# Optimization experiments

Measured on AMD Instinct MI355X. Metric: run time of the kernel, lower is better.

The kernel has to match this reference:

```python
import jax, jax.numpy as jnp
import numpy as np

SCALING = 2.0  # lora alpha / r

def setup_inputs() -> dict:
    key = jax.random.key(0)
    k1, k2, k3, k4, k5 = jax.random.split(key, 5)
    B, S, D_IN, D_OUT, R = 4, 2048, 4096, 4096, 16
    x = jax.random.normal(k1, (B, S, D_IN), dtype=jnp.float32)
    weight = jax.random.normal(k2, (D_OUT, D_IN), dtype=jnp.float32) * 0.02
    lora_A = jax.random.normal(k3, (R, D_IN), dtype=jnp.float32) * (1.0 / np.sqrt(D_IN))
    lora_B = jax.random.normal(k4, (D_OUT, R), dtype=jnp.float32) * 0.02
    bias = jax.random.normal(k5, (D_OUT,), dtype=jnp.float32) * 0.02
    return {"x": x, "weight": weight, "lora_A": lora_A, "lora_B": lora_B, "bias": bias}

def reference(x, weight, lora_A, lora_B, bias):
    # Faithful to the torch module: materialize W + scaling * (B @ A), then F.linear.
    # effective_weight: [d_out, d_in]
    effective_weight = weight + SCALING * (lora_B @ lora_A)
    # F.linear(x, W, b) = x @ W.T + b
    out = jnp.einsum('bsd,od->bso', x, effective_weight) + bias
    return out
```

## Files before the change

kernel.cpp:

```cpp
#include <hip/hip_runtime.h>
#include <hip/hip_bf16.h>
#include <stdint.h>

typedef unsigned short u16;
typedef u16 u16x4 __attribute__((ext_vector_type(4)));
typedef short bf16x8 __attribute__((ext_vector_type(8)));
typedef float f32x4 __attribute__((ext_vector_type(4)));

__device__ __forceinline__ u16 f2bf(float f) {
  union { float f; uint32_t u; } v; v.f = f;
  uint32_t u = v.u;
  return (u16)((u + 0x7fffu + ((u >> 16) & 1u)) >> 16);
}

__global__ __launch_bounds__(256) void cvt_x_kernel(const float4* __restrict__ in,
                                                    u16x4* __restrict__ out, int n4) {
  int i = blockIdx.x * 256 + threadIdx.x;
  const int stride = gridDim.x * 256;
  for (; i < n4; i += stride) {
    float4 v = in[i];
    u16x4 o;
    o.x = f2bf(v.x); o.y = f2bf(v.y); o.z = f2bf(v.z); o.w = f2bf(v.w);
    out[i] = o;
  }
}

__global__ __launch_bounds__(256) void weff_kernel(const float* __restrict__ W,
                                                   const float* __restrict__ A,
                                                   const float* __restrict__ Bl,
                                                   u16* __restrict__ Wout, int DIN) {
  const int n = blockIdx.x;
  float bv[16];
#pragma unroll
  for (int r = 0; r < 16; ++r) bv[r] = 2.0f * Bl[n * 16 + r];
  const int iters = DIN / (256 * 4);
  for (int c = 0; c < iters; ++c) {
    const int k = (c * 256 + (int)threadIdx.x) * 4;
    float4 wv = *(const float4*)&W[(size_t)n * DIN + k];
#pragma unroll
    for (int r = 0; r < 16; ++r) {
      const float4 av = *(const float4*)&A[(size_t)r * DIN + k];
      wv.x += bv[r] * av.x;
      wv.y += bv[r] * av.y;
      wv.z += bv[r] * av.z;
      wv.w += bv[r] * av.w;
    }
    u16x4 o;
    o.x = f2bf(wv.x); o.y = f2bf(wv.y); o.z = f2bf(wv.z); o.w = f2bf(wv.w);
    *(u16x4*)&Wout[(size_t)n * DIN + k] = o;
  }
}

#define BM 256
#define BN 256

__global__ __launch_bounds__(512, 2) void gemm256_kernel(
    const u16* __restrict__ A, const u16* __restrict__ B,
    const float* __restrict__ bias, float* __restrict__ C,
    int M, int N, int K) {
  extern __shared__ u16 lds[];

  const int tid  = threadIdx.x;
  const int lane = tid & 63;
  const int wid  = tid >> 6;

  const int nwg = gridDim.x;
  const int cpx = nwg >> 3;
  const int f   = ((int)blockIdx.x & 7) * cpx + ((int)blockIdx.x >> 3);
  const int nbx = N / BN;
  const int bx = f % nbx, by = f / nbx;
  const int bm = by * BM, bn = bx * BN;

  const int wmL = (wid >> 2) * 128;
  const int wnL = (wid & 3) * 64;
  const int lr  = lane & 15;
  const int lk  = lane >> 4;
  const int rslot = ((lk ^ ((lr >> 1) & 3)) << 3);

  const int srow  = tid >> 2;
  const int sslot = (((tid & 3) ^ ((tid >> 3) & 3)) << 3);
  const u16* gA = A + (size_t)(bm + srow) * K + sslot;
  const u16* gB = B + (size_t)(bn + srow) * K + sslot;

  auto stageA = [&](int par, int ks, int kt) {
    u16* d = &lds[(par * 2 + ks) * 8192 + wid * 512];
    const u16* s = gA + kt * 64 + ks * 32;
#pragma unroll
    for (int i = 0; i < 2; ++i)
      __builtin_amdgcn_global_load_lds(
          (__attribute__((address_space(1))) const void*)(s + (size_t)i * 128 * K),
          (__attribute__((address_space(3))) void*)(d + i * 4096), 16, 0, 0);
  };
  auto stageB = [&](int par, int ks, int kt) {
    u16* d = &lds[32768 + (par * 2 + ks) * 8192 + wid * 512];
    const u16* s = gB + kt * 64 + ks * 32;
#pragma unroll
    for (int i = 0; i < 2; ++i)
      __builtin_amdgcn_global_load_lds(
          (__attribute__((address_space(1))) const void*)(s + (size_t)i * 128 * K),
          (__attribute__((address_space(3))) void*)(d + i * 4096), 16, 0, 0);
  };

  f32x4 acc[8][4];
#pragma unroll
  for (int i = 0; i < 8; ++i)
#pragma unroll
    for (int n = 0; n < 4; ++n) acc[i][n] = f32x4{0.f, 0.f, 0.f, 0.f};

  const int NT = K >> 6;
  stageA(0, 0, 0); stageB(0, 0, 0); stageA(0, 1, 0); stageB(0, 1, 0);

#define GATE4() do { asm volatile("s_waitcnt vmcnt(4)" ::: "memory"); \
                     __builtin_amdgcn_s_barrier(); } while (0)

  for (int t = 0; t < NT; ++t) {
    const int par = t & 1, npar = par ^ 1;
    const int tn = (t + 1 < NT) ? t + 1 : 0;

    auto ldA = [&](int ks, int mf) -> bf16x8 {
      return *(const bf16x8*)&lds[(par * 2 + ks) * 8192 + (wmL + mf * 16 + lr) * 32 + rslot];
    };
    auto ldB = [&](int ks, int nf) -> bf16x8 {
      return *(const bf16x8*)&lds[32768 + (par * 2 + ks) * 8192 + (wnL + nf * 16 + lr) * 32 + rslot];
    };

    bf16x8 a[4], b0[4], b1[4];

    GATE4();
#pragma unroll
    for (int n = 0; n < 4; ++n) b0[n] = ldB(0, n);
#pragma unroll
    for (int i = 0; i < 4; ++i) a[i] = ldA(0, i);
    stageA(npar, 0, tn);
    __builtin_amdgcn_s_setprio(1);
#pragma unroll
    for (int i = 0; i < 4; ++i)
#pragma unroll
      for (int n = 0; n < 4; ++n)
        acc[i][n] = __builtin_amdgcn_mfma_f32_16x16x32_bf16(a[i], b0[n], acc[i][n], 0, 0, 0);
    __builtin_amdgcn_s_setprio(0);

#pragma unroll
    for (int i = 0; i < 4; ++i) a[i] = ldA(0, 4 + i);
    stageB(npar, 0, tn);
    __builtin_amdgcn_s_setprio(1);
#pragma unroll
    for (int i = 0; i < 4; ++i)
#pragma unroll
      for (int n = 0; n < 4; ++n)
        acc[4 + i][n] = __builtin_amdgcn_mfma_f32_16x16x32_bf16(a[i], b0[n], acc[4 + i][n], 0, 0, 0);
    __builtin_amdgcn_s_setprio(0);

    GATE4();
#pragma unroll
    for (int n = 0; n < 4; ++n) b1[n] = ldB(1, n);
#pragma unroll
    for (int i = 0; i < 4; ++i) a[i] = ldA(1, i);
    stageA(npar, 1, tn);
    __builtin_amdgcn_s_setprio(1);
#pragma unroll
    for (int i = 0; i < 4; ++i)
#pragma unroll
      for (int n = 0; n < 4; ++n)
        acc[i][n] = __builtin_amdgcn_mfma_f32_16x16x32_bf16(a[i], b1[n], acc[i][n], 0, 0, 0);
    __builtin_amdgcn_s_setprio(0);

#pragma unroll
    for (int i = 0; i < 4; ++i) a[i] = ldA(1, 4 + i);
    stageB(npar, 1, tn);
    __builtin_amdgcn_s_setprio(1);
#pragma unroll
    for (int i = 0; i < 4; ++i)
#pragma unroll
      for (int n = 0; n < 4; ++n)
        acc[4 + i][n] = __builtin_amdgcn_mfma_f32_16x16x32_bf16(a[i], b1[n], acc[4 + i][n], 0, 0, 0);
    __builtin_amdgcn_s_setprio(0);
  }

  asm volatile("s_waitcnt vmcnt(0)" ::: "memory");
  __builtin_amdgcn_s_barrier();

#pragma unroll
  for (int nf = 0; nf < 4; ++nf) {
    const int col = bn + wnL + nf * 16 + lr;
    const float bv = bias[col];
#pragma unroll
    for (int mf = 0; mf < 8; ++mf) {
      const int row = bm + wmL + mf * 16 + lk * 4;
#pragma unroll
      for (int j = 0; j < 4; ++j)
        C[(size_t)(row + j) * N + col] = acc[mf][nf][j] + bv;
    }
  }
}

extern "C" void kernel_launch(void* const* d_in, const int* in_sizes, int n_in,
                              void* d_out, int out_size, void* d_ws, size_t ws_size,
                              hipStream_t stream) {
  const float* x  = (const float*)d_in[0];
  const float* w  = (const float*)d_in[1];
  const float* lA = (const float*)d_in[2];
  const float* lB = (const float*)d_in[3];
  const float* bs = (const float*)d_in[4];
  float* out = (float*)d_out;

  const int DOUT = in_sizes[4];
  const int DIN  = in_sizes[1] / DOUT;
  const int M    = in_sizes[0] / DIN;

  u16* Xb = (u16*)d_ws;
  u16* Wb = Xb + (size_t)M * DIN;

  const int n4 = (M * DIN) / 4;
  cvt_x_kernel<<<2048, 256, 0, stream>>>((const float4*)x, (u16x4*)Xb, n4);
  weff_kernel<<<DOUT, 256, 0, stream>>>(w, lA, lB, Wb, DIN);

  static bool attr_set = false;
  (void)hipFuncSetAttribute((const void*)gemm256_kernel,
                            hipFuncAttributeMaxDynamicSharedMemorySize, 131072);

  const int nwg = (M / BM) * (DOUT / BN);
  gemm256_kernel<<<nwg, 512, 131072, stream>>>(Xb, Wb, bs, out, M, DOUT, DIN);
}
```

Baseline: 342.3 us.

## Merge prep kernels and restructure GEMM barrier schedule per sub-phase

Merges the x-to-bf16 conversion and effective-weight kernels into one launch, with blocks split by index, to remove a launch and let the two prep tasks run concurrently. In the GEMM main loop, it replaces the two vmcnt-gated barriers per k-tile with a barrier after every LDS-read/stage group and after every MFMA cluster, plus an lgkmcnt(0) wait before each MFMA block. The intent is to keep waves in lockstep so MFMA and memory phases interleave better across waves. The cost is many more barriers per iteration, which could add stalls.

```diff
diff --git a/kernel.cpp b/kernel.cpp
--- a/kernel.cpp
+++ b/kernel.cpp
@@ -13,41 +13,40 @@
   return (u16)((u + 0x7fffu + ((u >> 16) & 1u)) >> 16);
 }
 
-__global__ __launch_bounds__(256) void cvt_x_kernel(const float4* __restrict__ in,
-                                                    u16x4* __restrict__ out, int n4) {
-  int i = blockIdx.x * 256 + threadIdx.x;
-  const int stride = gridDim.x * 256;
-  for (; i < n4; i += stride) {
-    float4 v = in[i];
-    u16x4 o;
-    o.x = f2bf(v.x); o.y = f2bf(v.y); o.z = f2bf(v.z); o.w = f2bf(v.w);
-    out[i] = o;
-  }
-}
-
-__global__ __launch_bounds__(256) void weff_kernel(const float* __restrict__ W,
-                                                   const float* __restrict__ A,
-                                                   const float* __restrict__ Bl,
-                                                   u16* __restrict__ Wout, int DIN) {
-  const int n = blockIdx.x;
-  float bv[16];
-#pragma unroll
-  for (int r = 0; r < 16; ++r) bv[r] = 2.0f * Bl[n * 16 + r];
-  const int iters = DIN / (256 * 4);
-  for (int c = 0; c < iters; ++c) {
-    const int k = (c * 256 + (int)threadIdx.x) * 4;
-    float4 wv = *(const float4*)&W[(size_t)n * DIN + k];
-#pragma unroll
-    for (int r = 0; r < 16; ++r) {
-      const float4 av = *(const float4*)&A[(size_t)r * DIN + k];
-      wv.x += bv[r] * av.x;
-      wv.y += bv[r] * av.y;
-      wv.z += bv[r] * av.z;
-      wv.w += bv[r] * av.w;
+__global__ __launch_bounds__(256) void aux_kernel(
+    const float4* __restrict__ x, u16x4* __restrict__ xb, int n4, int nCvt,
+    const float* __restrict__ W, const float* __restrict__ A,
+    const float* __restrict__ Bl, u16* __restrict__ Wout, int DIN) {
+  if ((int)blockIdx.x < nCvt) {
+    int i = blockIdx.x * 256 + threadIdx.x;
+    const int stride = nCvt * 256;
+    for (; i < n4; i += stride) {
+      float4 v = x[i];
+      u16x4 o;
+      o.x = f2bf(v.x); o.y = f2bf(v.y); o.z = f2bf(v.z); o.w = f2bf(v.w);
+      xb[i] = o;
     }
-    u16x4 o;
-    o.x = f2bf(wv.x); o.y = f2bf(wv.y); o.z = f2bf(wv.z); o.w = f2bf(wv.w);
-    *(u16x4*)&Wout[(size_t)n * DIN + k] = o;
+  } else {
+    const int n = blockIdx.x - nCvt;
+    float bv[16];
+#pragma unroll
+    for (int r = 0; r < 16; ++r) bv[r] = 2.0f * Bl[n * 16 + r];
+    const int iters = DIN / (256 * 4);
+    for (int c = 0; c < iters; ++c) {
+      const int k = (c * 256 + (int)threadIdx.x) * 4;
+      float4 wv = *(const float4*)&W[(size_t)n * DIN + k];
+#pragma unroll
+      for (int r = 0; r < 16; ++r) {
+        const float4 av = *(const float4*)&A[(size_t)r * DIN + k];
+        wv.x += bv[r] * av.x;
+        wv.y += bv[r] * av.y;
+        wv.z += bv[r] * av.z;
+        wv.w += bv[r] * av.w;
+      }
+      u16x4 o;
+      o.x = f2bf(wv.x); o.y = f2bf(wv.y); o.z = f2bf(wv.z); o.w = f2bf(wv.w);
+      *(u16x4*)&Wout[(size_t)n * DIN + k] = o;
+    }
   }
 }
 
@@ -109,9 +108,13 @@
 
   const int NT = K >> 6;
   stageA(0, 0, 0); stageB(0, 0, 0); stageA(0, 1, 0); stageB(0, 1, 0);
-
-#define GATE4() do { asm volatile("s_waitcnt vmcnt(4)" ::: "memory"); \
-                     __builtin_amdgcn_s_barrier(); } while (0)
+  asm volatile("s_waitcnt vmcnt(4)" ::: "memory");
+  __builtin_amdgcn_s_barrier();
+
+#define PIN()   asm volatile("" ::: "memory")
+#define LGKM0() asm volatile("s_waitcnt lgkmcnt(0)" ::: "memory")
+#define VM4()   asm volatile("s_waitcnt vmcnt(4)" ::: "memory")
+#define BAR()   __builtin_amdgcn_s_barrier()
 
   for (int t = 0; t < NT; ++t) {
     const int par = t & 1, npar = par ^ 1;
@@ -126,12 +129,12 @@
 
     bf16x8 a[4], b0[4], b1[4];
 
-    GATE4();
 #pragma unroll
     for (int n = 0; n < 4; ++n) b0[n] = ldB(0, n);
 #pragma unroll
     for (int i = 0; i < 4; ++i) a[i] = ldA(0, i);
     stageA(npar, 0, tn);
+    PIN(); BAR(); LGKM0();
     __builtin_amdgcn_s_setprio(1);
 #pragma unroll
     for (int i = 0; i < 4; ++i)
@@ -139,10 +142,12 @@
       for (int n = 0; n < 4; ++n)
         acc[i][n] = __builtin_amdgcn_mfma_f32_16x16x32_bf16(a[i], b0[n], acc[i][n], 0, 0, 0);
     __builtin_amdgcn_s_setprio(0);
+    BAR();
 
 #pragma unroll
     for (int i = 0; i < 4; ++i) a[i] = ldA(0, 4 + i);
     stageB(npar, 0, tn);
+    PIN(); BAR(); LGKM0();
     __builtin_amdgcn_s_setprio(1);
 #pragma unroll
     for (int i = 0; i < 4; ++i)
@@ -150,13 +155,15 @@
       for (int n = 0; n < 4; ++n)
         acc[4 + i][n] = __builtin_amdgcn_mfma_f32_16x16x32_bf16(a[i], b0[n], acc[4 + i][n], 0, 0, 0);
     __builtin_amdgcn_s_setprio(0);
-
-    GATE4();
+    VM4();
+    BAR();
+
 #pragma unroll
     for (int n = 0; n < 4; ++n) b1[n] = ldB(1, n);
 #pragma unroll
     for (int i = 0; i < 4; ++i) a[i] = ldA(1, i);
     stageA(npar, 1, tn);
+    PIN(); BAR(); LGKM0();
     __builtin_amdgcn_s_setprio(1);
 #pragma unroll
     for (int i = 0; i < 4; ++i)
@@ -164,10 +171,12 @@
       for (int n = 0; n < 4; ++n)
         acc[i][n] = __builtin_amdgcn_mfma_f32_16x16x32_bf16(a[i], b1[n], acc[i][n], 0, 0, 0);
     __builtin_amdgcn_s_setprio(0);
+    BAR();
 
 #pragma unroll
     for (int i = 0; i < 4; ++i) a[i] = ldA(1, 4 + i);
     stageB(npar, 1, tn);
+    PIN(); BAR(); LGKM0();
     __builtin_amdgcn_s_setprio(1);
 #pragma unroll
     for (int i = 0; i < 4; ++i)
@@ -175,6 +184,8 @@
       for (int n = 0; n < 4; ++n)
         acc[4 + i][n] = __builtin_amdgcn_mfma_f32_16x16x32_bf16(a[i], b1[n], acc[4 + i][n], 0, 0, 0);
     __builtin_amdgcn_s_setprio(0);
+    VM4();
+    BAR();
   }
 
   asm volatile("s_waitcnt vmcnt(0)" ::: "memory");
@@ -192,6 +203,10 @@
         C[(size_t)(row + j) * N + col] = acc[mf][nf][j] + bv;
     }
   }
+#undef PIN
+#undef LGKM0
+#undef VM4
+#undef BAR
 }
 
 extern "C" void kernel_launch(void* const* d_in, const int* in_sizes, int n_in,
@@ -212,10 +227,10 @@
   u16* Wb = Xb + (size_t)M * DIN;
 
   const int n4 = (M * DIN) / 4;
-  cvt_x_kernel<<<2048, 256, 0, stream>>>((const float4*)x, (u16x4*)Xb, n4);
-  weff_kernel<<<DOUT, 256, 0, stream>>>(w, lA, lB, Wb, DIN);
-
-  static bool attr_set = false;
+  const int nCvt = 2048;
+  aux_kernel<<<nCvt + DOUT, 256, 0, stream>>>((const float4*)x, (u16x4*)Xb, n4, nCvt,
+                                              w, lA, lB, Wb, DIN);
+
   (void)hipFuncSetAttribute((const void*)gemm256_kernel,
                             hipFuncAttributeMaxDynamicSharedMemorySize, 131072);
 
```

Measured after the change: 341.8 us. About the same (-0.2%).

## Switch GEMM to 32x32x16 MFMA and merge preprocessing kernels into one launch

Applied to the files above, without the earlier changes.

The main GEMM now uses 32x32x16 bf16 MFMA instructions with 32-row fragments instead of 16x16x32. This halves the number of MFMA issues and LDS fragment reads per tile and changes the LDS read swizzle and the output write pattern. The x-to-bf16 conversion and the effective-weight kernels are merged into a single launch. The weight path now handles 8 output rows per block and reuses the loaded lora_A values across those rows. Risks include a new LDS bank-conflict pattern, more strided output stores, and register pressure from holding 16 float4 values of A.

```diff
diff --git a/kernel.cpp b/kernel.cpp
--- a/kernel.cpp
+++ b/kernel.cpp
@@ -6,6 +6,7 @@
 typedef u16 u16x4 __attribute__((ext_vector_type(4)));
 typedef short bf16x8 __attribute__((ext_vector_type(8)));
 typedef float f32x4 __attribute__((ext_vector_type(4)));
+typedef float f32x16 __attribute__((ext_vector_type(16)));
 
 __device__ __forceinline__ u16 f2bf(float f) {
   union { float f; uint32_t u; } v; v.f = f;
@@ -13,41 +14,44 @@
   return (u16)((u + 0x7fffu + ((u >> 16) & 1u)) >> 16);
 }
 
-__global__ __launch_bounds__(256) void cvt_x_kernel(const float4* __restrict__ in,
-                                                    u16x4* __restrict__ out, int n4) {
-  int i = blockIdx.x * 256 + threadIdx.x;
-  const int stride = gridDim.x * 256;
-  for (; i < n4; i += stride) {
-    float4 v = in[i];
-    u16x4 o;
-    o.x = f2bf(v.x); o.y = f2bf(v.y); o.z = f2bf(v.z); o.w = f2bf(v.w);
-    out[i] = o;
-  }
-}
-
-__global__ __launch_bounds__(256) void weff_kernel(const float* __restrict__ W,
-                                                   const float* __restrict__ A,
-                                                   const float* __restrict__ Bl,
-                                                   u16* __restrict__ Wout, int DIN) {
-  const int n = blockIdx.x;
-  float bv[16];
-#pragma unroll
-  for (int r = 0; r < 16; ++r) bv[r] = 2.0f * Bl[n * 16 + r];
-  const int iters = DIN / (256 * 4);
-  for (int c = 0; c < iters; ++c) {
-    const int k = (c * 256 + (int)threadIdx.x) * 4;
-    float4 wv = *(const float4*)&W[(size_t)n * DIN + k];
-#pragma unroll
-    for (int r = 0; r < 16; ++r) {
-      const float4 av = *(const float4*)&A[(size_t)r * DIN + k];
-      wv.x += bv[r] * av.x;
-      wv.y += bv[r] * av.y;
-      wv.z += bv[r] * av.z;
-      wv.w += bv[r] * av.w;
+__global__ __launch_bounds__(256) void aux_kernel(
+    const float4* __restrict__ x, u16x4* __restrict__ xb, int n4, int nCvt,
+    const float* __restrict__ W, const float* __restrict__ A,
+    const float* __restrict__ Bl, u16* __restrict__ Wout, int DIN) {
+  if ((int)blockIdx.x < nCvt) {
+    int i = blockIdx.x * 256 + threadIdx.x;
+    const int stride = nCvt * 256;
+    for (; i < n4; i += stride) {
+      float4 v = x[i];
+      u16x4 o;
+      o.x = f2bf(v.x); o.y = f2bf(v.y); o.z = f2bf(v.z); o.w = f2bf(v.w);
+      xb[i] = o;
     }
-    u16x4 o;
-    o.x = f2bf(wv.x); o.y = f2bf(wv.y); o.z = f2bf(wv.z); o.w = f2bf(wv.w);
-    *(u16x4*)&Wout[(size_t)n * DIN + k] = o;
+  } else {
+    const int n0 = ((int)blockIdx.x - nCvt) * 8;
+    const int iters = DIN / (256 * 4);
+    for (int c = 0; c < iters; ++c) {
+      const int k = (c * 256 + (int)threadIdx.x) * 4;
+      float4 av[16];
+#pragma unroll
+      for (int r = 0; r < 16; ++r) av[r] = *(const float4*)&A[(size_t)r * DIN + k];
+#pragma unroll
+      for (int nn = 0; nn < 8; ++nn) {
+        const int n = n0 + nn;
+        float4 wv = *(const float4*)&W[(size_t)n * DIN + k];
+#pragma unroll
+        for (int r = 0; r < 16; ++r) {
+          const float bv = 2.0f * Bl[n * 16 + r];
+          wv.x += bv * av[r].x;
+          wv.y += bv * av[r].y;
+          wv.z += bv * av[r].z;
+          wv.w += bv * av[r].w;
+        }
+        u16x4 o;
+        o.x = f2bf(wv.x); o.y = f2bf(wv.y); o.z = f2bf(wv.z); o.w = f2bf(wv.w);
+        *(u16x4*)&Wout[(size_t)n * DIN + k] = o;
+      }
+    }
   }
 }
 
@@ -73,27 +77,29 @@
 
   const int wmL = (wid >> 2) * 128;
   const int wnL = (wid & 3) * 64;
-  const int lr  = lane & 15;
-  const int lk  = lane >> 4;
-  const int rslot = ((lk ^ ((lr >> 1) & 3)) << 3);
+  const int l31 = lane & 31;
+  const int l5  = lane >> 5;
+  const int swz = (l31 >> 1) & 3;
+  const int ks8_0 = ((0 * 2 + l5) ^ swz) << 3;
+  const int ks8_1 = ((1 * 2 + l5) ^ swz) << 3;
 
   const int srow  = tid >> 2;
   const int sslot = (((tid & 3) ^ ((tid >> 3) & 3)) << 3);
   const u16* gA = A + (size_t)(bm + srow) * K + sslot;
   const u16* gB = B + (size_t)(bn + srow) * K + sslot;
 
-  auto stageA = [&](int par, int ks, int kt) {
-    u16* d = &lds[(par * 2 + ks) * 8192 + wid * 512];
-    const u16* s = gA + kt * 64 + ks * 32;
+  auto stageA = [&](int par, int kp, int kt) {
+    u16* d = &lds[(par * 2 + kp) * 8192 + wid * 512];
+    const u16* s = gA + kt * 64 + kp * 32;
 #pragma unroll
     for (int i = 0; i < 2; ++i)
       __builtin_amdgcn_global_load_lds(
           (__attribute__((address_space(1))) const void*)(s + (size_t)i * 128 * K),
           (__attribute__((address_space(3))) void*)(d + i * 4096), 16, 0, 0);
   };
-  auto stageB = [&](int par, int ks, int kt) {
-    u16* d = &lds[32768 + (par * 2 + ks) * 8192 + wid * 512];
-    const u16* s = gB + kt * 64 + ks * 32;
+  auto stageB = [&](int par, int kp, int kt) {
+    u16* d = &lds[32768 + (par * 2 + kp) * 8192 + wid * 512];
+    const u16* s = gB + kt * 64 + kp * 32;
 #pragma unroll
     for (int i = 0; i < 2; ++i)
       __builtin_amdgcn_global_load_lds(
@@ -101,11 +107,13 @@
           (__attribute__((address_space(3))) void*)(d + i * 4096), 16, 0, 0);
   };
 
-  f32x4 acc[8][4];
-#pragma unroll
-  for (int i = 0; i < 8; ++i)
-#pragma unroll
-    for (int n = 0; n < 4; ++n) acc[i][n] = f32x4{0.f, 0.f, 0.f, 0.f};
+  f32x16 acc[4][2];
+#pragma unroll
+  for (int i = 0; i < 4; ++i)
+#pragma unroll
+    for (int n = 0; n < 2; ++n)
+#pragma unroll
+      for (int r = 0; r < 16; ++r) acc[i][n][r] = 0.f;
 
   const int NT = K >> 6;
   stageA(0, 0, 0); stageB(0, 0, 0); stageA(0, 1, 0); stageB(0, 1, 0);
@@ -117,63 +125,85 @@
     const int par = t & 1, npar = par ^ 1;
     const int tn = (t + 1 < NT) ? t + 1 : 0;
 
-    auto ldA = [&](int ks, int mf) -> bf16x8 {
-      return *(const bf16x8*)&lds[(par * 2 + ks) * 8192 + (wmL + mf * 16 + lr) * 32 + rslot];
+    auto ldA = [&](int kp, int s, int mf) -> bf16x8 {
+      return *(const bf16x8*)&lds[(par * 2 + kp) * 8192 +
+                                  (wmL + mf * 32 + l31) * 32 + (s ? ks8_1 : ks8_0)];
     };
-    auto ldB = [&](int ks, int nf) -> bf16x8 {
-      return *(const bf16x8*)&lds[32768 + (par * 2 + ks) * 8192 + (wnL + nf * 16 + lr) * 32 + rslot];
+    auto ldB = [&](int kp, int s, int nf) -> bf16x8 {
+      return *(const bf16x8*)&lds[32768 + (par * 2 + kp) * 8192 +
+                                  (wnL + nf * 32 + l31) * 32 + (s ? ks8_1 : ks8_0)];
     };
 
-    bf16x8 a[4], b0[4], b1[4];
+    bf16x8 a[2][2], b[2][2];
 
     GATE4();
 #pragma unroll
-    for (int n = 0; n < 4; ++n) b0[n] = ldB(0, n);
-#pragma unroll
-    for (int i = 0; i < 4; ++i) a[i] = ldA(0, i);
+    for (int s = 0; s < 2; ++s)
+#pragma unroll
+      for (int n = 0; n < 2; ++n) b[s][n] = ldB(0, s, n);
+#pragma unroll
+    for (int s = 0; s < 2; ++s)
+#pragma unroll
+      for (int m = 0; m < 2; ++m) a[s][m] = ldA(0, s, m);
     stageA(npar, 0, tn);
     __builtin_amdgcn_s_setprio(1);
 #pragma unroll
-    for (int i = 0; i < 4; ++i)
-#pragma unroll
-      for (int n = 0; n < 4; ++n)
-        acc[i][n] = __builtin_amdgcn_mfma_f32_16x16x32_bf16(a[i], b0[n], acc[i][n], 0, 0, 0);
-    __builtin_amdgcn_s_setprio(0);
-
-#pragma unroll
-    for (int i = 0; i < 4; ++i) a[i] = ldA(0, 4 + i);
+    for (int s = 0; s < 2; ++s)
+#pragma unroll
+      for (int m = 0; m < 2; ++m)
+#pragma unroll
+        for (int n = 0; n < 2; ++n)
+          acc[m][n] = __builtin_amdgcn_mfma_f32_32x32x16_bf16(a[s][m], b[s][n], acc[m][n], 0, 0, 0);
+    __builtin_amdgcn_s_setprio(0);
+
+#pragma unroll
+    for (int s = 0; s < 2; ++s)
+#pragma unroll
+      for (int m = 0; m < 2; ++m) a[s][m] = ldA(0, s, 2 + m);
     stageB(npar, 0, tn);
     __builtin_amdgcn_s_setprio(1);
 #pragma unroll
-    for (int i = 0; i < 4; ++i)
-#pragma unroll
-      for (int n = 0; n < 4; ++n)
-        acc[4 + i][n] = __builtin_amdgcn_mfma_f32_16x16x32_bf16(a[i], b0[n], acc[4 + i][n], 0, 0, 0);
+    for (int s = 0; s < 2; ++s)
+#pragma unroll
+      for (int m = 0; m < 2; ++m)
+#pragma unroll
+        for (int n = 0; n < 2; ++n)
+          acc[2 + m][n] = __builtin_amdgcn_mfma_f32_32x32x16_bf16(a[s][m], b[s][n], acc[2 + m][n], 0, 0, 0);
     __builtin_amdgcn_s_setprio(0);
 
     GATE4();
 #pragma unroll
-    for (int n = 0; n < 4; ++n) b1[n] = ldB(1, n);
-#pragma unroll
-    for (int i = 0; i < 4; ++i) a[i] = ldA(1, i);
+    for (int s = 0; s < 2; ++s)
+#pragma unroll
+      for (int n = 0; n < 2; ++n) b[s][n] = ldB(1, s, n);
+#pragma unroll
+    for (int s = 0; s < 2; ++s)
+#pragma unroll
+      for (int m = 0; m < 2; ++m) a[s][m] = ldA(1, s, m);
     stageA(npar, 1, tn);
     __builtin_amdgcn_s_setprio(1);
 #pragma unroll
-    for (int i = 0; i < 4; ++i)
-#pragma unroll
-      for (int n = 0; n < 4; ++n)
-        acc[i][n] = __builtin_amdgcn_mfma_f32_16x16x32_bf16(a[i], b1[n], acc[i][n], 0, 0, 0);
-    __builtin_amdgcn_s_setprio(0);
-
-#pragma unroll
-    for (int i = 0; i < 4; ++i) a[i] = ldA(1, 4 + i);
+    for (int s = 0; s < 2; ++s)
+#pragma unroll
+      for (int m = 0; m < 2; ++m)
+#pragma unroll
+        for (int n = 0; n < 2; ++n)
+          acc[m][n] = __builtin_amdgcn_mfma_f32_32x32x16_bf16(a[s][m], b[s][n], acc[m][n], 0, 0, 0);
+    __builtin_amdgcn_s_setprio(0);
+
+#pragma unroll
+    for (int s = 0; s < 2; ++s)
+#pragma unroll
+      for (int m = 0; m < 2; ++m) a[s][m] = ldA(1, s, 2 + m);
     stageB(npar, 1, tn);
     __builtin_amdgcn_s_setprio(1);
 #pragma unroll
-    for (int i = 0; i < 4; ++i)
-#pragma unroll
-      for (int n = 0; n < 4; ++n)
-        acc[4 + i][n] = __builtin_amdgcn_mfma_f32_16x16x32_bf16(a[i], b1[n], acc[4 + i][n], 0, 0, 0);
+    for (int s = 0; s < 2; ++s)
+#pragma unroll
+      for (int m = 0; m < 2; ++m)
+#pragma unroll
+        for (int n = 0; n < 2; ++n)
+          acc[2 + m][n] = __builtin_amdgcn_mfma_f32_32x32x16_bf16(a[s][m], b[s][n], acc[2 + m][n], 0, 0, 0);
     __builtin_amdgcn_s_setprio(0);
   }
 
@@ -181,17 +211,20 @@
   __builtin_amdgcn_s_barrier();
 
 #pragma unroll
-  for (int nf = 0; nf < 4; ++nf) {
-    const int col = bn + wnL + nf * 16 + lr;
+  for (int nf = 0; nf < 2; ++nf) {
+    const int col = bn + wnL + nf * 32 + l31;
     const float bv = bias[col];
 #pragma unroll
-    for (int mf = 0; mf < 8; ++mf) {
-      const int row = bm + wmL + mf * 16 + lk * 4;
-#pragma unroll
-      for (int j = 0; j < 4; ++j)
-        C[(size_t)(row + j) * N + col] = acc[mf][nf][j] + bv;
+    for (int mf = 0; mf < 4; ++mf) {
+      const int rowbase = bm + wmL + mf * 32 + 4 * l5;
+#pragma unroll
+      for (int r = 0; r < 16; ++r) {
+        const int row = rowbase + (r & 3) + 8 * (r >> 2);
+        C[(size_t)row * N + col] = acc[mf][nf][r] + bv;
+      }
     }
   }
+#undef GATE4
 }
 
 extern "C" void kernel_launch(void* const* d_in, const int* in_sizes, int n_in,
@@ -212,10 +245,11 @@
   u16* Wb = Xb + (size_t)M * DIN;
 
   const int n4 = (M * DIN) / 4;
-  cvt_x_kernel<<<2048, 256, 0, stream>>>((const float4*)x, (u16x4*)Xb, n4);
-  weff_kernel<<<DOUT, 256, 0, stream>>>(w, lA, lB, Wb, DIN);
-
-  static bool attr_set = false;
+  const int nCvt = 2048;
+  const int nWeff = DOUT / 8;
+  aux_kernel<<<nCvt + nWeff, 256, 0, stream>>>((const float4*)x, (u16x4*)Xb, n4, nCvt,
+                                               w, lA, lB, Wb, DIN);
+
   (void)hipFuncSetAttribute((const void*)gemm256_kernel,
                             hipFuncAttributeMaxDynamicSharedMemorySize, 131072);
 
```

After: 397.5 us. 16.1% more time.
